# Kernel tuning notes

Measured on AMD Instinct MI355X. Metric: run time of the kernel, lower is better.

## Reference

```python
import jax, jax.numpy as jnp
import numpy as np

N_VAR, N_CONS, E = 50000, 50000, 800000
F, FE, H, ITERS = 64, 8, 128, 2  # node feat, edge feat, hidden, gnn iterations


def _mlp(x, w1, b1, w2, b2):
    # MultilayerPerceptron([in, hidden, out]) = Linear -> ReLU -> Linear
    return jax.nn.relu(x @ w1 + b1) @ w2 + b2


def setup_inputs() -> dict:
    key = jax.random.key(0)
    ks = jax.random.split(key, 17)

    def w(k, shape, fan_in):
        return jax.random.normal(k, shape, jnp.float32) / np.sqrt(fan_in).astype(np.float32)

    msg_in = 2 * F + FE   # 136
    upd_in = 2 * F        # 128
    return {
        "var_feat": jax.random.normal(ks[0], (N_VAR, F), jnp.float32),
        "cons_feat": jax.random.normal(ks[1], (N_CONS, F), jnp.float32),
        "edge_feat": jax.random.normal(ks[2], (E, FE), jnp.float32),
        "edge_var": jax.random.randint(ks[3], (E,), 0, N_VAR),
        "edge_cons": jax.random.randint(ks[4], (E,), 0, N_CONS),
        # messenger MLP (note: original code uses var messenger for BOTH sides)
        "w_msg1": w(ks[5], (ITERS, msg_in, H), msg_in),
        "b_msg1": jnp.zeros((ITERS, H), jnp.float32),
        "w_msg2": w(ks[6], (ITERS, H, F), H),
        "b_msg2": jnp.zeros((ITERS, F), jnp.float32),
        # var update MLP
        "w_vupd1": w(ks[7], (ITERS, upd_in, H), upd_in),
        "b_vupd1": jnp.zeros((ITERS, H), jnp.float32),
        "w_vupd2": w(ks[8], (ITERS, H, F), H),
        "b_vupd2": jnp.zeros((ITERS, F), jnp.float32),
        # cons update MLP
        "w_cupd1": w(ks[9], (ITERS, upd_in, H), upd_in),
        "b_cupd1": jnp.zeros((ITERS, H), jnp.float32),
        "w_cupd2": w(ks[10], (ITERS, H, F), H),
        "b_cupd2": jnp.zeros((ITERS, F), jnp.float32),
    }


def reference(var_feat, cons_feat, edge_feat, edge_var, edge_cons,
              w_msg1, b_msg1, w_msg2, b_msg2,
              w_vupd1, b_vupd1, w_vupd2, b_vupd2,
              w_cupd1, b_cupd1, w_cupd2, b_cupd2):
    for i in range(ITERS):
        vs = var_feat[edge_var]    # [E, F] gather of var endpoint feats
        cs = cons_feat[edge_cons]  # [E, F] gather of cons endpoint feats
        # --- var-node message pass: (var_feat, neighbor cons_feat, edge_feat) ---
        m_v = _mlp(jnp.concatenate([vs, cs, edge_feat], axis=1),
                   w_msg1[i], b_msg1[i], w_msg2[i], b_msg2[i])        # [E, F]
        agg_v = jax.ops.segment_sum(m_v, edge_var, num_segments=N_VAR)  # zeros for isolated nodes
        new_var = _mlp(jnp.concatenate([var_feat, agg_v], axis=1),
                       w_vupd1[i], b_vupd1[i], w_vupd2[i], b_vupd2[i])
        # --- cons-node message pass (uses var messenger weights, as in source) ---
        m_c = _mlp(jnp.concatenate([cs, vs, edge_feat], axis=1),
                   w_msg1[i], b_msg1[i], w_msg2[i], b_msg2[i])        # [E, F]
        agg_c = jax.ops.segment_sum(m_c, edge_cons, num_segments=N_CONS)
        new_cons = _mlp(jnp.concatenate([cons_feat, agg_c], axis=1),
                        w_cupd1[i], b_cupd1[i], w_cupd2[i], b_cupd2[i])
        var_feat, cons_feat = new_var, new_cons
    return var_feat, cons_feat
```

## Files before the change

kernel.cpp:

```cpp
#include <hip/hip_runtime.h>

#define N_NODES 50000
#define E_EDGES 800000
#define F 64
#define FE 8
#define H 128
#define MSG_IN 136
#define XPAD 168
#define HPW 68
#define NXP 136

typedef short bf16x8 __attribute__((ext_vector_type(8)));
typedef float f32x4 __attribute__((ext_vector_type(4)));

__device__ __forceinline__ ushort f2bf(float f) {
  uint u = __float_as_uint(f);
  u = (u + 0x7FFFu + ((u >> 16) & 1u)) >> 16;
  return (ushort)u;
}
__device__ __forceinline__ uint pack2(float lo, float hi) {
  uint r;
  asm("v_cvt_pk_bf16_f32 %0, %1, %2" : "=v"(r) : "v"(lo), "v"(hi));
  return r;
}
__device__ __forceinline__ void atomic_pk_add_bf16(ushort* addr, uint data) {
  asm volatile("global_atomic_pk_add_bf16 %0, %1, off" :: "v"(addr), "v"(data) : "memory");
}

__global__ __launch_bounds__(256)
void cvt_feats(const float* __restrict__ a, const float* __restrict__ b,
               ushort* __restrict__ oa, ushort* __restrict__ ob) {
  const int n4 = N_NODES * F / 4;
  for (int i = blockIdx.x * blockDim.x + threadIdx.x; i < n4; i += gridDim.x * blockDim.x) {
    const float4 va = ((const float4*)a)[i];
    const float4 vb = ((const float4*)b)[i];
    ((uint2*)oa)[i] = make_uint2(pack2(va.x, va.y), pack2(va.z, va.w));
    ((uint2*)ob)[i] = make_uint2(pack2(vb.x, vb.y), pack2(vb.z, vb.w));
  }
}

__global__ __launch_bounds__(256, 2)
void edge_pass_mfma(const ushort* __restrict__ vfeat, const ushort* __restrict__ cfeat,
                    const float* __restrict__ efeat,
                    const int* __restrict__ ev, const int* __restrict__ ec,
                    const float* __restrict__ w1, const float* __restrict__ b1,
                    const float* __restrict__ w2, const float* __restrict__ b2,
                    ushort* __restrict__ aggv, ushort* __restrict__ aggc)
{
  __shared__ __align__(16) ushort sX[64 * XPAD];
  __shared__ __align__(16) uint  sH[128 * HPW];
  __shared__ int sIv[64], sIc[64];

  const int t = threadIdx.x;
  const int wid = t >> 6, l15 = t & 15, hi = (t >> 4) & 3;
  const int eh = wid >> 1, fh = wid & 1;

  bf16x8 bf1[2][5];
  #pragma unroll
  for (int n = 0; n < 2; ++n) {
    const int col = wid * 32 + n * 16 + l15;
    #pragma unroll
    for (int kb = 0; kb < 5; ++kb)
      #pragma unroll
      for (int i = 0; i < 8; ++i) {
        const int kg = kb * 32 + hi * 8 + i;
        float val = 0.f;
        if (kg < MSG_IN) val = w1[kg * H + col];
        else if (kg == MSG_IN) val = b1[col];
        bf1[n][kb][i] = (short)f2bf(val);
      }
  }
  bf16x8 bf2[2][4];
  #pragma unroll
  for (int fbl = 0; fbl < 2; ++fbl) {
    const int col = fh * 32 + 2 * l15 + fbl;
    #pragma unroll
    for (int kb = 0; kb < 4; ++kb)
      #pragma unroll
      for (int i = 0; i < 8; ++i) {
        const int p = hi * 8 + i;
        const int kl = (p >> 1) | ((p & 1) << 4);
        bf2[fbl][kb][i] = (short)f2bf(w2[(kb * 32 + kl) * F + col]);
      }
  }
  const float bb2[2] = { b2[fh * 32 + 2 * l15], b2[fh * 32 + 2 * l15 + 1] };

  {
    uint* xu = (uint*)sX;
    for (int i = t; i < 64 * 16; i += 256) {
      const int row = i >> 4, u = i & 15;
      xu[row * (XPAD / 2) + 68 + u] = (u == 0) ? 0x00003F80u : 0u;
    }
  }

  const int r = t >> 2, q = t & 3;
  const int g = gridDim.x;
  const int nTiles = E_EDGES / 64;
  int tile = blockIdx.x;

  constexpr int perm[5] = {2, 3, 0, 1, 4};

  int ivC = ev[tile * 64 + r], icC = ec[tile * 64 + r];
  {
    const int nt = (tile + g < nTiles) ? tile + g : tile;
    const uint4* vp = (const uint4*)(vfeat + (size_t)ivC * F);
    const uint4* cp = (const uint4*)(cfeat + (size_t)icC * F);
  }
  uint4 sv0, sv1, sc0, sc1;
  float4 fe0, fe1;
  {
    const uint4* vp = (const uint4*)(vfeat + (size_t)ivC * F);
    const uint4* cp = (const uint4*)(cfeat + (size_t)icC * F);
    sv0 = vp[q * 2]; sv1 = vp[q * 2 + 1];
    sc0 = cp[q * 2]; sc1 = cp[q * 2 + 1];
    if (q == 0) {
      const float4* ep = (const float4*)(efeat + (size_t)(tile * 64 + r) * FE);
      fe0 = ep[0]; fe1 = ep[1];
    }
  }
  int ivN, icN;
  {
    const int nt = (tile + g < nTiles) ? tile + g : tile;
    ivN = ev[nt * 64 + r]; icN = ec[nt * 64 + r];
  }

  for (; tile < nTiles; tile += g) {
    {
      uint4* xr4 = (uint4*)((uint*)sX + r * (XPAD / 2));
      xr4[q * 2]     = sv0;
      xr4[q * 2 + 1] = sv1;
      xr4[8 + q * 2]     = sc0;
      xr4[8 + q * 2 + 1] = sc1;
      if (q == 0)
        xr4[16] = make_uint4(pack2(fe0.x, fe0.y), pack2(fe0.z, fe0.w),
                             pack2(fe1.x, fe1.y), pack2(fe1.z, fe1.w));
    }
    __syncthreads();
    if (q == 0) { sIv[r] = ivC; sIc[r] = icC; }

    ivC = ivN; icC = icN;
    {
      const int t2 = (tile + 2 * g < nTiles) ? tile + 2 * g : tile;
      ivN = ev[t2 * 64 + r]; icN = ec[t2 * 64 + r];
      const uint4* vp = (const uint4*)(vfeat + (size_t)ivC * F);
      const uint4* cp = (const uint4*)(cfeat + (size_t)icC * F);
      sv0 = vp[q * 2]; sv1 = vp[q * 2 + 1];
      sc0 = cp[q * 2]; sc1 = cp[q * 2 + 1];
      if (q == 0) {
        const int en = ((tile + g < nTiles) ? tile + g : tile) * 64 + r;
        const float4* ep = (const float4*)(efeat + (size_t)en * FE);
        fe0 = ep[0]; fe1 = ep[1];
      }
    }

    f32x4 acc[4][2];

    #pragma unroll
    for (int m = 0; m < 4; ++m)
      #pragma unroll
      for (int n = 0; n < 2; ++n) acc[m][n] = (f32x4)(0.f);
    #pragma unroll
    for (int kb = 0; kb < 5; ++kb)
      #pragma unroll
      for (int m = 0; m < 4; ++m) {
        const bf16x8 a = *(const bf16x8*)&sX[(m * 16 + l15) * XPAD + kb * 32 + hi * 8];
        #pragma unroll
        for (int n = 0; n < 2; ++n)
          acc[m][n] = __builtin_amdgcn_mfma_f32_16x16x32_bf16(a, bf1[n][kb], acc[m][n], 0, 0, 0);
      }
    #pragma unroll
    for (int m = 0; m < 4; ++m)
      #pragma unroll
      for (int rr = 0; rr < 4; ++rr) {
        const int e = m * 16 + hi * 4 + rr;
        sH[e * HPW + wid * 16 + l15] =
            pack2(fmaxf(acc[m][0][rr], 0.f), fmaxf(acc[m][1][rr], 0.f));
      }

    #pragma unroll
    for (int m = 0; m < 4; ++m)
      #pragma unroll
      for (int n = 0; n < 2; ++n) acc[m][n] = (f32x4)(0.f);
    #pragma unroll
    for (int kb = 0; kb < 5; ++kb)
      #pragma unroll
      for (int m = 0; m < 4; ++m) {
        const bf16x8 a = *(const bf16x8*)&sX[(m * 16 + l15) * XPAD + kb * 32 + hi * 8];
        #pragma unroll
        for (int n = 0; n < 2; ++n)
          acc[m][n] = __builtin_amdgcn_mfma_f32_16x16x32_bf16(a, bf1[n][perm[kb]], acc[m][n], 0, 0, 0);
      }
    #pragma unroll
    for (int m = 0; m < 4; ++m)
      #pragma unroll
      for (int rr = 0; rr < 4; ++rr) {
        const int e = m * 16 + hi * 4 + rr;
        sH[(64 + e) * HPW + wid * 16 + l15] =
            pack2(fmaxf(acc[m][0][rr], 0.f), fmaxf(acc[m][1][rr], 0.f));
      }
    __syncthreads();

    const ushort* sHu = (const ushort*)sH;
    #pragma unroll
    for (int side = 0; side < 2; ++side) {
      f32x4 a2[2][2];
      #pragma unroll
      for (int mm = 0; mm < 2; ++mm) { a2[mm][0] = (f32x4)(0.f); a2[mm][1] = (f32x4)(0.f); }
      #pragma unroll
      for (int kb = 0; kb < 4; ++kb)
        #pragma unroll
        for (int mm = 0; mm < 2; ++mm) {
          const int e = side * 64 + (eh * 2 + mm) * 16 + l15;
          const bf16x8 a = *(const bf16x8*)&sHu[e * (HPW * 2) + kb * 32 + hi * 8];
          a2[mm][0] = __builtin_amdgcn_mfma_f32_16x16x32_bf16(a, bf2[0][kb], a2[mm][0], 0, 0, 0);
          a2[mm][1] = __builtin_amdgcn_mfma_f32_16x16x32_bf16(a, bf2[1][kb], a2[mm][1], 0, 0, 0);
        }
      ushort* agg = side ? aggc : aggv;
      const int* sI = side ? sIc : sIv;
      #pragma unroll
      for (int mm = 0; mm < 2; ++mm)
        #pragma unroll
        for (int rr = 0; rr < 4; ++rr) {
          const int idx = sI[(eh * 2 + mm) * 16 + hi * 4 + rr];
          ushort* dst = agg + (size_t)idx * F + fh * 32 + 2 * l15;
          atomic_pk_add_bf16(dst, pack2(a2[mm][0][rr] + bb2[0], a2[mm][1][rr] + bb2[1]));
        }
    }
  }
}

__global__ __launch_bounds__(256, 2)
void node_update_dual(ushort* __restrict__ vfeat, const ushort* __restrict__ vagg,
                      ushort* __restrict__ cfeat, const ushort* __restrict__ cagg,
                      const float* __restrict__ w1v, const float* __restrict__ b1v,
                      const float* __restrict__ w2v, const float* __restrict__ b2v,
                      const float* __restrict__ w1c, const float* __restrict__ b1c,
                      const float* __restrict__ w2c, const float* __restrict__ b2c,
                      float* __restrict__ outv, float* __restrict__ outc,
                      int writeF32)
{
  __shared__ __align__(16) ushort sX[64 * NXP];
  __shared__ __align__(16) uint  sH[64 * HPW];

  const int half = (N_NODES + 63) / 64;
  const bool isC = (int)blockIdx.x >= half;
  const int tile = isC ? blockIdx.x - half : blockIdx.x;
  ushort* feat = isC ? cfeat : vfeat;
  const ushort* agg = isC ? cagg : vagg;
  const float* w1 = isC ? w1c : w1v;  const float* b1 = isC ? b1c : b1v;
  const float* w2 = isC ? w2c : w2v;  const float* b2 = isC ? b2c : b2v;
  float* outf = isC ? outc : outv;

  const int t = threadIdx.x;
  const int wid = t >> 6, l15 = t & 15, hi = (t >> 4) & 3;

  bf16x8 bf1[2][4];
  #pragma unroll
  for (int n = 0; n < 2; ++n) {
    const int col = wid * 32 + n * 16 + l15;
    #pragma unroll
    for (int kb = 0; kb < 4; ++kb)
      #pragma unroll
      for (int i = 0; i < 8; ++i)
        bf1[n][kb][i] = (short)f2bf(w1[(kb * 32 + hi * 8 + i) * H + col]);
  }
  bf16x8 bf2[2][2][4];
  #pragma unroll
  for (int gg = 0; gg < 2; ++gg)
    #pragma unroll
    for (int fbl = 0; fbl < 2; ++fbl) {
      const int col = gg * 32 + 2 * l15 + fbl;
      #pragma unroll
      for (int kb = 0; kb < 4; ++kb)
        #pragma unroll
        for (int i = 0; i < 8; ++i) {
          const int p = hi * 8 + i;
          const int kl = (p >> 1) | ((p & 1) << 4);
          bf2[gg][fbl][kb][i] = (short)f2bf(w2[(kb * 32 + kl) * F + col]);
        }
    }
  const float bb1[2] = { b1[wid * 32 + l15], b1[wid * 32 + 16 + l15] };
  float bb2[2][2];
  #pragma unroll
  for (int gg = 0; gg < 2; ++gg) {
    bb2[gg][0] = b2[gg * 32 + 2 * l15];
    bb2[gg][1] = b2[gg * 32 + 2 * l15 + 1];
  }

  const int r = t >> 2, q = t & 3;
  {
    const int node = tile * 64 + r;
    const int nc = node < N_NODES ? node : N_NODES - 1;
    const uint4* fp = (const uint4*)(feat + (size_t)nc * F);
    const uint4* ap = (const uint4*)(agg + (size_t)nc * F);
    uint4* xr4 = (uint4*)&sX[r * NXP];
    xr4[q * 2]     = fp[q * 2];
    xr4[q * 2 + 1] = fp[q * 2 + 1];
    xr4[8 + q * 2]     = ap[q * 2];
    xr4[8 + q * 2 + 1] = ap[q * 2 + 1];
  }
  __syncthreads();

  f32x4 aV[4][2];
  #pragma unroll
  for (int m = 0; m < 4; ++m)
    #pragma unroll
    for (int n = 0; n < 2; ++n) aV[m][n] = (f32x4)(0.f);
  #pragma unroll
  for (int kb = 0; kb < 4; ++kb)
    #pragma unroll
    for (int m = 0; m < 4; ++m) {
      const bf16x8 a = *(const bf16x8*)&sX[(m * 16 + l15) * NXP + kb * 32 + hi * 8];
      #pragma unroll
      for (int n = 0; n < 2; ++n)
        aV[m][n] = __builtin_amdgcn_mfma_f32_16x16x32_bf16(a, bf1[n][kb], aV[m][n], 0, 0, 0);
    }
  #pragma unroll
  for (int m = 0; m < 4; ++m)
    #pragma unroll
    for (int rr = 0; rr < 4; ++rr) {
      const int e = m * 16 + hi * 4 + rr;
      sH[e * HPW + wid * 16 + l15] =
          pack2(fmaxf(aV[m][0][rr] + bb1[0], 0.f), fmaxf(aV[m][1][rr] + bb1[1], 0.f));
    }
  __syncthreads();

  f32x4 a2[2][2];
  #pragma unroll
  for (int gg = 0; gg < 2; ++gg)
    #pragma unroll
    for (int fbl = 0; fbl < 2; ++fbl) a2[gg][fbl] = (f32x4)(0.f);
  const ushort* sHu = (const ushort*)sH;
  #pragma unroll
  for (int kb = 0; kb < 4; ++kb) {
    const int e = wid * 16 + l15;
    const bf16x8 a = *(const bf16x8*)&sHu[e * (HPW * 2) + kb * 32 + hi * 8];
    #pragma unroll
    for (int gg = 0; gg < 2; ++gg)
      #pragma unroll
      for (int fbl = 0; fbl < 2; ++fbl)
        a2[gg][fbl] = __builtin_amdgcn_mfma_f32_16x16x32_bf16(a, bf2[gg][fbl][kb], a2[gg][fbl], 0, 0, 0);
  }
  #pragma unroll
  for (int rr = 0; rr < 4; ++rr) {
    const int node = tile * 64 + wid * 16 + hi * 4 + rr;
    if (node < N_NODES) {
      #pragma unroll
      for (int gg = 0; gg < 2; ++gg) {
        const float o0 = a2[gg][0][rr] + bb2[gg][0];
        const float o1 = a2[gg][1][rr] + bb2[gg][1];
        *(uint*)&feat[(size_t)node * F + gg * 32 + 2 * l15] = pack2(o0, o1);
        if (writeF32) {
          float2 o = make_float2(o0, o1);
          *(float2*)&outf[(size_t)node * F + gg * 32 + 2 * l15] = o;
        }
      }
    }
  }
}

extern "C" void kernel_launch(void* const* d_in, const int* in_sizes, int n_in,
                              void* d_out, int out_size, void* d_ws, size_t ws_size,
                              hipStream_t stream) {
  const float* var_feat  = (const float*)d_in[0];
  const float* cons_feat = (const float*)d_in[1];
  const float* edge_feat = (const float*)d_in[2];
  const int*   ev        = (const int*)d_in[3];
  const int*   ec        = (const int*)d_in[4];
  const float* w_msg1  = (const float*)d_in[5];
  const float* b_msg1  = (const float*)d_in[6];
  const float* w_msg2  = (const float*)d_in[7];
  const float* b_msg2  = (const float*)d_in[8];
  const float* w_vupd1 = (const float*)d_in[9];
  const float* b_vupd1 = (const float*)d_in[10];
  const float* w_vupd2 = (const float*)d_in[11];
  const float* b_vupd2 = (const float*)d_in[12];
  const float* w_cupd1 = (const float*)d_in[13];
  const float* b_cupd1 = (const float*)d_in[14];
  const float* w_cupd2 = (const float*)d_in[15];
  const float* b_cupd2 = (const float*)d_in[16];

  const size_t NF = (size_t)N_NODES * F;
  ushort* aggv = (ushort*)d_ws;
  ushort* aggc = aggv + NF;
  ushort* vb   = aggc + NF;
  ushort* cb   = vb + NF;
  float* outv = (float*)d_out;
  float* outc = outv + NF;

  cvt_feats<<<512, 256, 0, stream>>>(var_feat, cons_feat, vb, cb);

  for (int it = 0; it < 2; ++it) {
    hipMemsetAsync(aggv, 0, 2 * NF * sizeof(ushort), stream);

    edge_pass_mfma<<<512, 256, 0, stream>>>(vb, cb, edge_feat, ev, ec,
        w_msg1 + (size_t)it * MSG_IN * H, b_msg1 + (size_t)it * H,
        w_msg2 + (size_t)it * H * F,      b_msg2 + (size_t)it * F,
        aggv, aggc);

    node_update_dual<<<1564, 256, 0, stream>>>(vb, aggv, cb, aggc,
        w_vupd1 + (size_t)it * H * H, b_vupd1 + (size_t)it * H,
        w_vupd2 + (size_t)it * H * F, b_vupd2 + (size_t)it * F,
        w_cupd1 + (size_t)it * H * H, b_cupd1 + (size_t)it * H,
        w_cupd2 + (size_t)it * H * F, b_cupd2 + (size_t)it * F,
        outv, outc, it == 1 ? 1 : 0);
  }
}
```

Measured before the change: 421.4 us.

## Sort edges by var index and merge same-node atomics in var aggregation

Adds a counting sort (histogram, single-block scan, scatter) that builds a permutation of edges ordered by var endpoint, run once per call. The edge pass then visits edges in that order, so consecutive rows in each MFMA output fragment often share a var index and their messages are summed in registers before a single packed bf16 atomic. This cuts var-side atomic traffic and contention and improves locality of var feature gathers, at the cost of three extra kernels, an indirect perm load, scattered edge_feat and ec reads, and cons-side atomics that are now less ordered. The scan runs on a single block, which may add serial latency.

```diff
diff --git a/kernel.cpp b/kernel.cpp
--- a/kernel.cpp
+++ b/kernel.cpp
@@ -39,10 +39,53 @@
   }
 }
 
+__global__ __launch_bounds__(256)
+void hist_kernel(const int* __restrict__ key, int* __restrict__ cnt) {
+  for (int e = blockIdx.x * blockDim.x + threadIdx.x; e < E_EDGES; e += gridDim.x * blockDim.x)
+    atomicAdd(&cnt[key[e]], 1);
+}
+
+__global__ __launch_bounds__(256)
+void scan_kernel(const int* __restrict__ cnt, int* __restrict__ off) {
+  __shared__ int part[256];
+  const int t = threadIdx.x;
+  const int CH = (N_NODES + 255) / 256;
+  int s = 0;
+  for (int j = 0; j < CH; ++j) {
+    const int idx = t * CH + j;
+    if (idx < N_NODES) s += cnt[idx];
+  }
+  part[t] = s;
+  __syncthreads();
+  for (int o = 1; o < 256; o <<= 1) {
+    int v = 0;
+    if (t >= o) v = part[t - o];
+    __syncthreads();
+    if (t >= o) part[t] += v;
+    __syncthreads();
+  }
+  int run = (t == 0) ? 0 : part[t - 1];
+  for (int j = 0; j < CH; ++j) {
+    const int idx = t * CH + j;
+    if (idx < N_NODES) { off[idx] = run; run += cnt[idx]; }
+  }
+}
+
+__global__ __launch_bounds__(256)
+void scatter_kernel(const int* __restrict__ key, const int* __restrict__ off,
+                    int* __restrict__ cnt2, int* __restrict__ perm) {
+  for (int e = blockIdx.x * blockDim.x + threadIdx.x; e < E_EDGES; e += gridDim.x * blockDim.x) {
+    const int n = key[e];
+    const int pos = off[n] + atomicAdd(&cnt2[n], 1);
+    perm[pos] = e;
+  }
+}
+
 __global__ __launch_bounds__(256, 2)
 void edge_pass_mfma(const ushort* __restrict__ vfeat, const ushort* __restrict__ cfeat,
                     const float* __restrict__ efeat,
                     const int* __restrict__ ev, const int* __restrict__ ec,
+                    const int* __restrict__ perm,
                     const float* __restrict__ w1, const float* __restrict__ b1,
                     const float* __restrict__ w2, const float* __restrict__ b2,
                     ushort* __restrict__ aggv, ushort* __restrict__ aggc)
@@ -98,14 +141,10 @@
   const int nTiles = E_EDGES / 64;
   int tile = blockIdx.x;
 
-  constexpr int perm[5] = {2, 3, 0, 1, 4};
-
-  int ivC = ev[tile * 64 + r], icC = ec[tile * 64 + r];
-  {
-    const int nt = (tile + g < nTiles) ? tile + g : tile;
-    const uint4* vp = (const uint4*)(vfeat + (size_t)ivC * F);
-    const uint4* cp = (const uint4*)(cfeat + (size_t)icC * F);
-  }
+  constexpr int perm5[5] = {2, 3, 0, 1, 4};
+
+  int pe = perm[tile * 64 + r];
+  int ivC = ev[pe], icC = ec[pe];
   uint4 sv0, sv1, sc0, sc1;
   float4 fe0, fe1;
   {
@@ -114,14 +153,15 @@
     sv0 = vp[q * 2]; sv1 = vp[q * 2 + 1];
     sc0 = cp[q * 2]; sc1 = cp[q * 2 + 1];
     if (q == 0) {
-      const float4* ep = (const float4*)(efeat + (size_t)(tile * 64 + r) * FE);
+      const float4* ep = (const float4*)(efeat + (size_t)pe * FE);
       fe0 = ep[0]; fe1 = ep[1];
     }
   }
-  int ivN, icN;
+  int peN, ivN, icN;
   {
     const int nt = (tile + g < nTiles) ? tile + g : tile;
-    ivN = ev[nt * 64 + r]; icN = ec[nt * 64 + r];
+    peN = perm[nt * 64 + r];
+    ivN = ev[peN]; icN = ec[peN];
   }
 
   for (; tile < nTiles; tile += g) {
@@ -138,17 +178,17 @@
     __syncthreads();
     if (q == 0) { sIv[r] = ivC; sIc[r] = icC; }
 
-    ivC = ivN; icC = icN;
+    ivC = ivN; icC = icN; pe = peN;
     {
       const int t2 = (tile + 2 * g < nTiles) ? tile + 2 * g : tile;
-      ivN = ev[t2 * 64 + r]; icN = ec[t2 * 64 + r];
+      peN = perm[t2 * 64 + r];
+      ivN = ev[peN]; icN = ec[peN];
       const uint4* vp = (const uint4*)(vfeat + (size_t)ivC * F);
       const uint4* cp = (const uint4*)(cfeat + (size_t)icC * F);
       sv0 = vp[q * 2]; sv1 = vp[q * 2 + 1];
       sc0 = cp[q * 2]; sc1 = cp[q * 2 + 1];
       if (q == 0) {
-        const int en = ((tile + g < nTiles) ? tile + g : tile) * 64 + r;
-        const float4* ep = (const float4*)(efeat + (size_t)en * FE);
+        const float4* ep = (const float4*)(efeat + (size_t)pe * FE);
         fe0 = ep[0]; fe1 = ep[1];
       }
     }
@@ -188,7 +228,7 @@
         const bf16x8 a = *(const bf16x8*)&sX[(m * 16 + l15) * XPAD + kb * 32 + hi * 8];
         #pragma unroll
         for (int n = 0; n < 2; ++n)
-          acc[m][n] = __builtin_amdgcn_mfma_f32_16x16x32_bf16(a, bf1[n][perm[kb]], acc[m][n], 0, 0, 0);
+          acc[m][n] = __builtin_amdgcn_mfma_f32_16x16x32_bf16(a, bf1[n][perm5[kb]], acc[m][n], 0, 0, 0);
       }
     #pragma unroll
     for (int m = 0; m < 4; ++m)
@@ -201,28 +241,61 @@
     __syncthreads();
 
     const ushort* sHu = (const ushort*)sH;
-    #pragma unroll
-    for (int side = 0; side < 2; ++side) {
+
+    {
       f32x4 a2[2][2];
       #pragma unroll
-      for (int mm = 0; mm < 2; ++mm) { a2[mm][0] = (f32x4)(0.f); a2[mm][1] = (f32x4)(0.f); }
+      for (int mm = 0; mm < 2; ++mm) {
+        a2[mm][0] = (f32x4)(bb2[0]);
+        a2[mm][1] = (f32x4)(bb2[1]);
+      }
       #pragma unroll
       for (int kb = 0; kb < 4; ++kb)
         #pragma unroll
         for (int mm = 0; mm < 2; ++mm) {
-          const int e = side * 64 + (eh * 2 + mm) * 16 + l15;
+          const int e = (eh * 2 + mm) * 16 + l15;
           const bf16x8 a = *(const bf16x8*)&sHu[e * (HPW * 2) + kb * 32 + hi * 8];
           a2[mm][0] = __builtin_amdgcn_mfma_f32_16x16x32_bf16(a, bf2[0][kb], a2[mm][0], 0, 0, 0);
           a2[mm][1] = __builtin_amdgcn_mfma_f32_16x16x32_bf16(a, bf2[1][kb], a2[mm][1], 0, 0, 0);
         }
-      ushort* agg = side ? aggc : aggv;
-      const int* sI = side ? sIc : sIv;
+      #pragma unroll
+      for (int mm = 0; mm < 2; ++mm) {
+        const int base = (eh * 2 + mm) * 16 + hi * 4;
+        int cur = sIv[base];
+        float s0 = a2[mm][0][0], s1 = a2[mm][1][0];
+        #pragma unroll
+        for (int rr = 1; rr < 4; ++rr) {
+          const int id = sIv[base + rr];
+          const float v0 = a2[mm][0][rr], v1 = a2[mm][1][rr];
+          if (id == cur) { s0 += v0; s1 += v1; }
+          else {
+            atomic_pk_add_bf16(aggv + (size_t)cur * F + fh * 32 + 2 * l15, pack2(s0, s1));
+            cur = id; s0 = v0; s1 = v1;
+          }
+        }
+        atomic_pk_add_bf16(aggv + (size_t)cur * F + fh * 32 + 2 * l15, pack2(s0, s1));
+      }
+    }
+
+    {
+      f32x4 a2[2][2];
+      #pragma unroll
+      for (int mm = 0; mm < 2; ++mm) { a2[mm][0] = (f32x4)(0.f); a2[mm][1] = (f32x4)(0.f); }
+      #pragma unroll
+      for (int kb = 0; kb < 4; ++kb)
+        #pragma unroll
+        for (int mm = 0; mm < 2; ++mm) {
+          const int e = 64 + (eh * 2 + mm) * 16 + l15;
+          const bf16x8 a = *(const bf16x8*)&sHu[e * (HPW * 2) + kb * 32 + hi * 8];
+          a2[mm][0] = __builtin_amdgcn_mfma_f32_16x16x32_bf16(a, bf2[0][kb], a2[mm][0], 0, 0, 0);
+          a2[mm][1] = __builtin_amdgcn_mfma_f32_16x16x32_bf16(a, bf2[1][kb], a2[mm][1], 0, 0, 0);
+        }
       #pragma unroll
       for (int mm = 0; mm < 2; ++mm)
         #pragma unroll
         for (int rr = 0; rr < 4; ++rr) {
-          const int idx = sI[(eh * 2 + mm) * 16 + hi * 4 + rr];
-          ushort* dst = agg + (size_t)idx * F + fh * 32 + 2 * l15;
+          const int idx = sIc[(eh * 2 + mm) * 16 + hi * 4 + rr];
+          ushort* dst = aggc + (size_t)idx * F + fh * 32 + 2 * l15;
           atomic_pk_add_bf16(dst, pack2(a2[mm][0][rr] + bb2[0], a2[mm][1][rr] + bb2[1]));
         }
     }
@@ -385,15 +458,25 @@
   ushort* aggc = aggv + NF;
   ushort* vb   = aggc + NF;
   ushort* cb   = vb + NF;
+  int* cnt  = (int*)(cb + NF);
+  int* off  = cnt + N_NODES;
+  int* cnt2 = off + N_NODES;
+  int* perm = cnt2 + N_NODES;
   float* outv = (float*)d_out;
   float* outc = outv + NF;
 
   cvt_feats<<<512, 256, 0, stream>>>(var_feat, cons_feat, vb, cb);
 
+  hipMemsetAsync(cnt, 0, 2 * N_NODES * sizeof(int), stream);
+  hipMemsetAsync(cnt2, 0, N_NODES * sizeof(int), stream);
+  hist_kernel<<<1024, 256, 0, stream>>>(ev, cnt);
+  scan_kernel<<<1, 256, 0, stream>>>(cnt, off);
+  scatter_kernel<<<1024, 256, 0, stream>>>(ev, off, cnt2, perm);
+
   for (int it = 0; it < 2; ++it) {
     hipMemsetAsync(aggv, 0, 2 * NF * sizeof(ushort), stream);
 
-    edge_pass_mfma<<<512, 256, 0, stream>>>(vb, cb, edge_feat, ev, ec,
+    edge_pass_mfma<<<512, 256, 0, stream>>>(vb, cb, edge_feat, ev, ec, perm,
         w_msg1 + (size_t)it * MSG_IN * H, b_msg1 + (size_t)it * H,
         w_msg2 + (size_t)it * H * F,      b_msg2 + (size_t)it * F,
         aggv, aggc);
```

Measured after the change: 618.1 us. 1.47x slower.
